# Performance work log

Measured on AMD Instinct MI355X. Metric: run time of the kernel, lower is better.

Reference implementation:

```python
import jax, jax.numpy as jnp
import numpy as np


def setup_inputs() -> dict:
    key = jax.random.key(0)
    k1, k2, k3 = jax.random.split(key, 3)
    B, L, D, H = 8, 1024, 768, 128
    text = jax.random.normal(k1, (B, L, D), dtype=jnp.float32)
    mask = jnp.ones((B, L), dtype=jnp.float32)  # accepted by forward but unused
    # nn.Linear-style init scale
    W0 = jax.random.normal(k2, (H, D), dtype=jnp.float32) / np.sqrt(D)
    b0 = jnp.zeros((H,), dtype=jnp.float32)
    W1 = jax.random.normal(k3, (1, 2 * H), dtype=jnp.float32) / np.sqrt(2 * H)
    b1 = jnp.zeros((1,), dtype=jnp.float32)
    return {"text": text, "mask": mask, "W0": W0, "b0": b0, "W1": W1, "b1": b1}


def reference(text, mask, W0, b0, W1, b1):
    # h = relu(linear0(text))  -> [B, L, 128]
    h = jax.nn.relu(jnp.einsum('bld,hd->blh', text, W0) + b0)
    H = W0.shape[0]
    # linear([h_i ; h_j]) = h_i @ w_a + h_j @ w_b + b  (split the 256->1 weight)
    w_a = W1[0, :H]   # weights applied to the row (i) copy
    w_b = W1[0, H:]   # weights applied to the column (j) copy
    s1 = jnp.einsum('blh,h->bl', h, w_a)  # [B, L]
    s2 = jnp.einsum('blh,h->bl', h, w_b)  # [B, L]
    # logits[b, i, j] = sigmoid(s1[b, i] + s2[b, j] + b1)
    logits = jax.nn.sigmoid(s1[:, :, None] + s2[:, None, :] + b1[0])
    return logits
```

## Files before the change

### kernel.cpp

```cpp
#include <hip/hip_runtime.h>

#define M_ROWS 8192
#define DIM    768
#define HCH    128

typedef __bf16 bf16x8 __attribute__((ext_vector_type(8)));
typedef float  f32x4  __attribute__((ext_vector_type(4)));

__device__ __forceinline__ unsigned short f2bf(float f) {
    union { float f; unsigned int u; } v; v.f = f;
    unsigned int u = v.u;
    u += 0x7fffu + ((u >> 16) & 1u);
    return (unsigned short)(u >> 16);
}
__device__ __forceinline__ unsigned int pk2bf(float x, float y) {
    return (unsigned int)f2bf(x) | ((unsigned int)f2bf(y) << 16);
}

__global__ __launch_bounds__(256) void gemm_s_kernel(
    const float* __restrict__ text,
    const float* __restrict__ W0,
    const float* __restrict__ b0,
    const float* __restrict__ W1,
    float* __restrict__ s1, float* __restrict__ s2)
{
    __shared__ unsigned short As[16][40];
    __shared__ unsigned short Bs[128][40];
    __shared__ float red1[16][4];
    __shared__ float red2[16][4];

    const int tid  = threadIdx.x;
    const int lane = tid & 63;
    const int wave = tid >> 6;
    const int row0 = blockIdx.x * 16;

    const int n16  = lane & 15;
    const int quad = lane >> 4;
    const int wcol = wave * 32;

    const int ar = tid >> 3;
    const int ak = (tid & 7) << 2;
    const int br = tid >> 1;
    const int bk = (tid & 1) << 4;

    const float* aptr = text + (size_t)(row0 + ar) * DIM + ak;
    const float* bptr = W0 + (size_t)br * DIM + bk;

    f32x4 acc[2];
    acc[0] = (f32x4){0.f, 0.f, 0.f, 0.f};
    acc[1] = (f32x4){0.f, 0.f, 0.f, 0.f};

    float4 av, bv[4];
    if (tid < 128) av = *(const float4*)aptr;
    #pragma unroll
    for (int q = 0; q < 4; ++q) bv[q] = *(const float4*)(bptr + q * 4);

    for (int kt = 0; kt < DIM; kt += 32) {
        const int ktn = (kt + 32 < DIM) ? (kt + 32) : 0;
        float4 av_n, bv_n[4];
        if (tid < 128) av_n = *(const float4*)(aptr + ktn);
        #pragma unroll
        for (int q = 0; q < 4; ++q) bv_n[q] = *(const float4*)(bptr + ktn + q * 4);

        if (tid < 128) {
            uint2 o;
            o.x = pk2bf(av.x, av.y);
            o.y = pk2bf(av.z, av.w);
            *(uint2*)&As[ar][ak] = o;
        }
        uint4 ob;
        ob.x = pk2bf(bv[0].x, bv[0].y);
        ob.y = pk2bf(bv[0].z, bv[0].w);
        ob.z = pk2bf(bv[1].x, bv[1].y);
        ob.w = pk2bf(bv[1].z, bv[1].w);
        *(uint4*)&Bs[br][bk] = ob;
        ob.x = pk2bf(bv[2].x, bv[2].y);
        ob.y = pk2bf(bv[2].z, bv[2].w);
        ob.z = pk2bf(bv[3].x, bv[3].y);
        ob.w = pk2bf(bv[3].z, bv[3].w);
        *(uint4*)&Bs[br][bk + 8] = ob;
        __syncthreads();

        bf16x8 a   = *(const bf16x8*)&As[n16][quad * 8];
        bf16x8 bf0 = *(const bf16x8*)&Bs[wcol +  0 + n16][quad * 8];
        bf16x8 bf1 = *(const bf16x8*)&Bs[wcol + 16 + n16][quad * 8];
        acc[0] = __builtin_amdgcn_mfma_f32_16x16x32_bf16(a, bf0, acc[0], 0, 0, 0);
        acc[1] = __builtin_amdgcn_mfma_f32_16x16x32_bf16(a, bf1, acc[1], 0, 0, 0);
        __syncthreads();

        av = av_n;
        #pragma unroll
        for (int q = 0; q < 4; ++q) bv[q] = bv_n[q];
    }

    float p1[4] = {0.f, 0.f, 0.f, 0.f};
    float p2[4] = {0.f, 0.f, 0.f, 0.f};
    #pragma unroll
    for (int j = 0; j < 2; ++j) {
        const int col = wcol + j * 16 + n16;
        const float bb = b0[col];
        const float wa = W1[col];
        const float wb = W1[HCH + col];
        #pragma unroll
        for (int r = 0; r < 4; ++r) {
            float h = acc[j][r] + bb;
            h = fmaxf(h, 0.f);
            p1[r] += h * wa;
            p2[r] += h * wb;
        }
    }
    #pragma unroll
    for (int r = 0; r < 4; ++r) {
        #pragma unroll
        for (int m = 8; m >= 1; m >>= 1) {
            p1[r] += __shfl_xor(p1[r], m);
            p2[r] += __shfl_xor(p2[r], m);
        }
    }
    if (n16 == 0) {
        #pragma unroll
        for (int r = 0; r < 4; ++r) {
            const int rr = quad * 4 + r;
            red1[rr][wave] = p1[r];
            red2[rr][wave] = p2[r];
        }
    }
    __syncthreads();
    if (tid < 16) {
        s1[row0 + tid] = red1[tid][0] + red1[tid][1] + red1[tid][2] + red1[tid][3];
        s2[row0 + tid] = red2[tid][0] + red2[tid][1] + red2[tid][2] + red2[tid][3];
    }
}

__global__ __launch_bounds__(256) void outer_sigmoid_kernel(
    const float* __restrict__ s1, const float* __restrict__ s2,
    const float* __restrict__ b1, float* __restrict__ out)
{
    const int bi = blockIdx.x;
    const int b  = bi >> 10;
    const float base = s1[bi] + b1[0];
    const float4 t = ((const float4*)(s2 + (b << 10)))[threadIdx.x];
    float4 r;
    r.x = 1.f / (1.f + __expf(-(base + t.x)));
    r.y = 1.f / (1.f + __expf(-(base + t.y)));
    r.z = 1.f / (1.f + __expf(-(base + t.z)));
    r.w = 1.f / (1.f + __expf(-(base + t.w)));
    ((float4*)out)[((size_t)bi << 8) + threadIdx.x] = r;
}

extern "C" void kernel_launch(void* const* d_in, const int* in_sizes, int n_in,
                              void* d_out, int out_size, void* d_ws, size_t ws_size,
                              hipStream_t stream)
{
    const float* text = (const float*)d_in[0];
    const float* W0 = (const float*)d_in[2];
    const float* b0 = (const float*)d_in[3];
    const float* W1 = (const float*)d_in[4];
    const float* b1 = (const float*)d_in[5];
    float* out = (float*)d_out;

    float* s1 = (float*)d_ws;
    float* s2 = s1 + M_ROWS;

    gemm_s_kernel<<<512, 256, 0, stream>>>(text, W0, b0, W1, s1, s2);
    outer_sigmoid_kernel<<<8192, 256, 0, stream>>>(s1, s2, b1, out);
}
```

Baseline: 104.1 us.

## Pre-convert W0 to bf16 once and widen GEMM K-tile to 64

Adds a small kernel that converts W0 to bf16 in workspace on every call, so each GEMM block loads half the weight bytes and skips per-block fp32-to-bf16 conversion. The K tile doubles to 64, which halves the number of loop iterations and barriers and lets all 256 threads load the A tile. The cost is an extra kernel launch plus an extra trip through global memory for the bf16 weights.

After: 145.3 us. 1.4x slower.

```diff
diff --git a/kernel.cpp b/kernel.cpp
--- a/kernel.cpp
+++ b/kernel.cpp
@@ -17,15 +17,26 @@
     return (unsigned int)f2bf(x) | ((unsigned int)f2bf(y) << 16);
 }
 
+__global__ __launch_bounds__(256) void convert_w0_kernel(
+    const float* __restrict__ W0, unsigned short* __restrict__ W0b)
+{
+    int i = (blockIdx.x * 256 + threadIdx.x) * 4;
+    float4 v = *(const float4*)(W0 + i);
+    uint2 o;
+    o.x = pk2bf(v.x, v.y);
+    o.y = pk2bf(v.z, v.w);
+    *(uint2*)(W0b + i) = o;
+}
+
 __global__ __launch_bounds__(256) void gemm_s_kernel(
     const float* __restrict__ text,
-    const float* __restrict__ W0,
+    const unsigned short* __restrict__ W0b,
     const float* __restrict__ b0,
     const float* __restrict__ W1,
     float* __restrict__ s1, float* __restrict__ s2)
 {
-    __shared__ unsigned short As[16][40];
-    __shared__ unsigned short Bs[128][40];
+    __shared__ unsigned short As[16][72];
+    __shared__ unsigned short Bs[128][72];
     __shared__ float red1[16][4];
     __shared__ float red2[16][4];
 
@@ -38,54 +49,54 @@
     const int quad = lane >> 4;
     const int wcol = wave * 32;
 
-    const int ar = tid >> 3;
-    const int ak = (tid & 7) << 2;
-    const int br = tid >> 1;
-    const int bk = (tid & 1) << 4;
+    const int ar = tid >> 4;
+    const int ak = (tid & 15) << 2;
+    const int br = tid >> 3;
+    const int bk = (tid & 7) << 3;
 
-    const float* aptr = text + (size_t)(row0 + ar) * DIM + ak;
-    const float* bptr = W0 + (size_t)br * DIM + bk;
+    const float*          aptr = text + (size_t)(row0 + ar) * DIM + ak;
+    const unsigned short* bptr = W0b + (size_t)br * DIM + bk;
 
     f32x4 acc[2];
     acc[0] = (f32x4){0.f, 0.f, 0.f, 0.f};
     acc[1] = (f32x4){0.f, 0.f, 0.f, 0.f};
 
-    float4 av, bv[4];
-    if (tid < 128) av = *(const float4*)aptr;
+    float4 av;
+    uint4  bv[4];
+    av = *(const float4*)aptr;
     #pragma unroll
-    for (int q = 0; q < 4; ++q) bv[q] = *(const float4*)(bptr + q * 4);
+    for (int q = 0; q < 4; ++q) bv[q] = *(const uint4*)(bptr + (size_t)q * 32 * DIM);
 
-    for (int kt = 0; kt < DIM; kt += 32) {
-        const int ktn = (kt + 32 < DIM) ? (kt + 32) : 0;
-        float4 av_n, bv_n[4];
-        if (tid < 128) av_n = *(const float4*)(aptr + ktn);
+    for (int kt = 0; kt < DIM; kt += 64) {
+        const int ktn = (kt + 64 < DIM) ? (kt + 64) : 0;
+        float4 av_n;
+        uint4  bv_n[4];
+        av_n = *(const float4*)(aptr + ktn);
         #pragma unroll
-        for (int q = 0; q < 4; ++q) bv_n[q] = *(const float4*)(bptr + ktn + q * 4);
+        for (int q = 0; q < 4; ++q)
+            bv_n[q] = *(const uint4*)(bptr + ktn + (size_t)q * 32 * DIM);
 
-        if (tid < 128) {
+        {
             uint2 o;
             o.x = pk2bf(av.x, av.y);
             o.y = pk2bf(av.z, av.w);
             *(uint2*)&As[ar][ak] = o;
         }
-        uint4 ob;
-        ob.x = pk2bf(bv[0].x, bv[0].y);
-        ob.y = pk2bf(bv[0].z, bv[0].w);
-        ob.z = pk2bf(bv[1].x, bv[1].y);
-        ob.w = pk2bf(bv[1].z, bv[1].w);
-        *(uint4*)&Bs[br][bk] = ob;
-        ob.x = pk2bf(bv[2].x, bv[2].y);
-        ob.y = pk2bf(bv[2].z, bv[2].w);
-        ob.z = pk2bf(bv[3].x, bv[3].y);
-        ob.w = pk2bf(bv[3].z, bv[3].w);
-        *(uint4*)&Bs[br][bk + 8] = ob;
+        #pragma unroll
+        for (int q = 0; q < 4; ++q)
+            *(uint4*)&Bs[br + q * 32][bk] = bv[q];
         __syncthreads();
 
-        bf16x8 a   = *(const bf16x8*)&As[n16][quad * 8];
-        bf16x8 bf0 = *(const bf16x8*)&Bs[wcol +  0 + n16][quad * 8];
-        bf16x8 bf1 = *(const bf16x8*)&Bs[wcol + 16 + n16][quad * 8];
-        acc[0] = __builtin_amdgcn_mfma_f32_16x16x32_bf16(a, bf0, acc[0], 0, 0, 0);
-        acc[1] = __builtin_amdgcn_mfma_f32_16x16x32_bf16(a, bf1, acc[1], 0, 0, 0);
+        bf16x8 a0 = *(const bf16x8*)&As[n16][quad * 8];
+        bf16x8 a1 = *(const bf16x8*)&As[n16][32 + quad * 8];
+        bf16x8 b00 = *(const bf16x8*)&Bs[wcol +  0 + n16][quad * 8];
+        bf16x8 b01 = *(const bf16x8*)&Bs[wcol +  0 + n16][32 + quad * 8];
+        bf16x8 b10 = *(const bf16x8*)&Bs[wcol + 16 + n16][quad * 8];
+        bf16x8 b11 = *(const bf16x8*)&Bs[wcol + 16 + n16][32 + quad * 8];
+        acc[0] = __builtin_amdgcn_mfma_f32_16x16x32_bf16(a0, b00, acc[0], 0, 0, 0);
+        acc[1] = __builtin_amdgcn_mfma_f32_16x16x32_bf16(a0, b10, acc[1], 0, 0, 0);
+        acc[0] = __builtin_amdgcn_mfma_f32_16x16x32_bf16(a1, b01, acc[0], 0, 0, 0);
+        acc[1] = __builtin_amdgcn_mfma_f32_16x16x32_bf16(a1, b11, acc[1], 0, 0, 0);
         __syncthreads();
 
         av = av_n;
@@ -159,9 +170,11 @@
     const float* b1 = (const float*)d_in[5];
     float* out = (float*)d_out;
 
-    float* s1 = (float*)d_ws;
+    unsigned short* W0b = (unsigned short*)d_ws;
+    float* s1 = (float*)((char*)d_ws + (size_t)HCH * DIM * sizeof(unsigned short));
     float* s2 = s1 + M_ROWS;
 
-    gemm_s_kernel<<<512, 256, 0, stream>>>(text, W0, b0, W1, s1, s2);
+    convert_w0_kernel<<<96, 256, 0, stream>>>(W0, W0b);
+    gemm_s_kernel<<<512, 256, 0, stream>>>(text, W0b, b0, W1, s1, s2);
     outer_sigmoid_kernel<<<8192, 256, 0, stream>>>(s1, s2, b1, out);
 }
```

## Pre-convert W0 to bf16 MFMA fragment layout and drop LDS staging

Applied to the files above, without the earlier changes.

Adds a small pre-pass kernel that converts W0 to bf16 and stores it in the exact per-lane MFMA fragment order. The GEMM kernel then loads its A and B fragments straight from global memory into registers through a 3-deep software pipeline, and no longer uses shared-memory tiles or per-step barriers. This removes the repeated fp32-to-bf16 conversion of W0 in every block and the LDS traffic and sync overhead. The cost is an extra kernel launch and uncoalesced-ish 32-byte text loads per lane.

New measurement: 102.5 us. About the same (-1.5%).

```diff
diff --git a/kernel.cpp b/kernel.cpp
--- a/kernel.cpp
+++ b/kernel.cpp
@@ -3,107 +3,96 @@
 #define M_ROWS 8192
 #define DIM    768
 #define HCH    128
+#define KSTEPS 24
 
 typedef __bf16 bf16x8 __attribute__((ext_vector_type(8)));
 typedef float  f32x4  __attribute__((ext_vector_type(4)));
 
-__device__ __forceinline__ unsigned short f2bf(float f) {
-    union { float f; unsigned int u; } v; v.f = f;
-    unsigned int u = v.u;
-    u += 0x7fffu + ((u >> 16) & 1u);
-    return (unsigned short)(u >> 16);
-}
-__device__ __forceinline__ unsigned int pk2bf(float x, float y) {
-    return (unsigned int)f2bf(x) | ((unsigned int)f2bf(y) << 16);
+__global__ __launch_bounds__(256) void convert_w0_frag(
+    const float* __restrict__ W0, bf16x8* __restrict__ W0f)
+{
+    const int g    = blockIdx.x * 256 + threadIdx.x;
+    const int c    = g / (KSTEPS * 64);
+    const int r    = g - c * (KSTEPS * 64);
+    const int s    = r >> 6;
+    const int lane = r & 63;
+    const int n16  = lane & 15;
+    const int quad = lane >> 4;
+    const float* src = W0 + (size_t)(c * 16 + n16) * DIM + s * 32 + quad * 8;
+    float4 v0 = *(const float4*)src;
+    float4 v1 = *(const float4*)(src + 4);
+    bf16x8 o;
+    o[0] = (__bf16)v0.x; o[1] = (__bf16)v0.y; o[2] = (__bf16)v0.z; o[3] = (__bf16)v0.w;
+    o[4] = (__bf16)v1.x; o[5] = (__bf16)v1.y; o[6] = (__bf16)v1.z; o[7] = (__bf16)v1.w;
+    W0f[g] = o;
 }
 
 __global__ __launch_bounds__(256) void gemm_s_kernel(
     const float* __restrict__ text,
-    const float* __restrict__ W0,
+    const bf16x8* __restrict__ W0f,
     const float* __restrict__ b0,
     const float* __restrict__ W1,
     float* __restrict__ s1, float* __restrict__ s2)
 {
-    __shared__ unsigned short As[16][40];
-    __shared__ unsigned short Bs[128][40];
     __shared__ float red1[16][4];
     __shared__ float red2[16][4];
 
     const int tid  = threadIdx.x;
     const int lane = tid & 63;
     const int wave = tid >> 6;
-    const int row0 = blockIdx.x * 16;
-
     const int n16  = lane & 15;
     const int quad = lane >> 4;
-    const int wcol = wave * 32;
+    const int row0 = blockIdx.x * 16;
+    const int c0   = wave * 2;
 
-    const int ar = tid >> 3;
-    const int ak = (tid & 7) << 2;
-    const int br = tid >> 1;
-    const int bk = (tid & 1) << 4;
+    const float*  aptr  = text + (size_t)(row0 + n16) * DIM + quad * 8;
+    const bf16x8* bptr0 = W0f + (size_t)(c0    ) * KSTEPS * 64 + lane;
+    const bf16x8* bptr1 = W0f + (size_t)(c0 + 1) * KSTEPS * 64 + lane;
 
-    const float* aptr = text + (size_t)(row0 + ar) * DIM + ak;
-    const float* bptr = W0 + (size_t)br * DIM + bk;
+    f32x4 acc0 = (f32x4){0.f, 0.f, 0.f, 0.f};
+    f32x4 acc1 = (f32x4){0.f, 0.f, 0.f, 0.f};
 
-    f32x4 acc[2];
-    acc[0] = (f32x4){0.f, 0.f, 0.f, 0.f};
-    acc[1] = (f32x4){0.f, 0.f, 0.f, 0.f};
+    float4 a0[3], a1[3];
+    bf16x8 bv0[3], bv1[3];
+    #pragma unroll
+    for (int s = 0; s < 2; ++s) {
+        a0[s]  = *(const float4*)(aptr + s * 32);
+        a1[s]  = *(const float4*)(aptr + s * 32 + 4);
+        bv0[s] = bptr0[s * 64];
+        bv1[s] = bptr1[s * 64];
+    }
 
-    float4 av, bv[4];
-    if (tid < 128) av = *(const float4*)aptr;
     #pragma unroll
-    for (int q = 0; q < 4; ++q) bv[q] = *(const float4*)(bptr + q * 4);
+    for (int s = 0; s < KSTEPS; ++s) {
+        const int sl = s % 3;
+        const int pl = (s + 2) % 3;
+        const int sp = (s + 2 < KSTEPS) ? (s + 2) : (s + 2 - KSTEPS);
+        a0[pl]  = *(const float4*)(aptr + sp * 32);
+        a1[pl]  = *(const float4*)(aptr + sp * 32 + 4);
+        bv0[pl] = bptr0[sp * 64];
+        bv1[pl] = bptr1[sp * 64];
 
-    for (int kt = 0; kt < DIM; kt += 32) {
-        const int ktn = (kt + 32 < DIM) ? (kt + 32) : 0;
-        float4 av_n, bv_n[4];
-        if (tid < 128) av_n = *(const float4*)(aptr + ktn);
-        #pragma unroll
-        for (int q = 0; q < 4; ++q) bv_n[q] = *(const float4*)(bptr + ktn + q * 4);
-
-        if (tid < 128) {
-            uint2 o;
-            o.x = pk2bf(av.x, av.y);
-            o.y = pk2bf(av.z, av.w);
-            *(uint2*)&As[ar][ak] = o;
-        }
-        uint4 ob;
-        ob.x = pk2bf(bv[0].x, bv[0].y);
-        ob.y = pk2bf(bv[0].z, bv[0].w);
-        ob.z = pk2bf(bv[1].x, bv[1].y);
-        ob.w = pk2bf(bv[1].z, bv[1].w);
-        *(uint4*)&Bs[br][bk] = ob;
-        ob.x = pk2bf(bv[2].x, bv[2].y);
-        ob.y = pk2bf(bv[2].z, bv[2].w);
-        ob.z = pk2bf(bv[3].x, bv[3].y);
-        ob.w = pk2bf(bv[3].z, bv[3].w);
-        *(uint4*)&Bs[br][bk + 8] = ob;
-        __syncthreads();
-
-        bf16x8 a   = *(const bf16x8*)&As[n16][quad * 8];
-        bf16x8 bf0 = *(const bf16x8*)&Bs[wcol +  0 + n16][quad * 8];
-        bf16x8 bf1 = *(const bf16x8*)&Bs[wcol + 16 + n16][quad * 8];
-        acc[0] = __builtin_amdgcn_mfma_f32_16x16x32_bf16(a, bf0, acc[0], 0, 0, 0);
-        acc[1] = __builtin_amdgcn_mfma_f32_16x16x32_bf16(a, bf1, acc[1], 0, 0, 0);
-        __syncthreads();
-
-        av = av_n;
-        #pragma unroll
-        for (int q = 0; q < 4; ++q) bv[q] = bv_n[q];
+        bf16x8 af;
+        af[0] = (__bf16)a0[sl].x; af[1] = (__bf16)a0[sl].y;
+        af[2] = (__bf16)a0[sl].z; af[3] = (__bf16)a0[sl].w;
+        af[4] = (__bf16)a1[sl].x; af[5] = (__bf16)a1[sl].y;
+        af[6] = (__bf16)a1[sl].z; af[7] = (__bf16)a1[sl].w;
+        acc0 = __builtin_amdgcn_mfma_f32_16x16x32_bf16(af, bv0[sl], acc0, 0, 0, 0);
+        acc1 = __builtin_amdgcn_mfma_f32_16x16x32_bf16(af, bv1[sl], acc1, 0, 0, 0);
     }
 
     float p1[4] = {0.f, 0.f, 0.f, 0.f};
     float p2[4] = {0.f, 0.f, 0.f, 0.f};
     #pragma unroll
     for (int j = 0; j < 2; ++j) {
-        const int col = wcol + j * 16 + n16;
+        const f32x4 aj = j ? acc1 : acc0;
+        const int col = wave * 32 + j * 16 + n16;
         const float bb = b0[col];
         const float wa = W1[col];
         const float wb = W1[HCH + col];
         #pragma unroll
         for (int r = 0; r < 4; ++r) {
-            float h = acc[j][r] + bb;
+            float h = aj[r] + bb;
             h = fmaxf(h, 0.f);
             p1[r] += h * wa;
             p2[r] += h * wb;
@@ -159,9 +148,11 @@
     const float* b1 = (const float*)d_in[5];
     float* out = (float*)d_out;
 
-    float* s1 = (float*)d_ws;
+    bf16x8* W0f = (bf16x8*)d_ws;
+    float* s1 = (float*)((char*)d_ws + (size_t)HCH * DIM * sizeof(unsigned short));
     float* s2 = s1 + M_ROWS;
 
-    gemm_s_kernel<<<512, 256, 0, stream>>>(text, W0, b0, W1, s1, s2);
+    convert_w0_frag<<<48, 256, 0, stream>>>(W0, W0f);
+    gemm_s_kernel<<<512, 256, 0, stream>>>(text, W0f, b0, W1, s1, s2);
     outer_sigmoid_kernel<<<8192, 256, 0, stream>>>(s1, s2, b1, out);
 }
```
